# Performance work log

Hardware: AMD Instinct MI355X
Metric: run time of the kernel (lower is better)

The kernel has to match this reference:

```python
import jax, jax.numpy as jnp
import numpy as np

N_DETS = 50000
K_NEIGH = 32
E = N_DETS * K_NEIGH  # 1,600,000 pairs


def _linear_params(key, fan_in, fan_out):
    kw, kb = jax.random.split(key)
    scale = 1.0 / np.sqrt(fan_in)
    W = jax.random.uniform(kw, (fan_in, fan_out), jnp.float32, -scale, scale)
    b = jax.random.uniform(kb, (fan_out,), jnp.float32, -scale, scale)
    return W, b


def setup_inputs() -> dict:
    key = jax.random.key(0)
    ks = jax.random.split(key, 10)
    detFeatures = jax.random.normal(ks[0], (N_DETS, 128), jnp.float32)
    # each detection is the center of exactly K_NEIGH pairs (sorted segment ids)
    cIdxs = jnp.repeat(jnp.arange(N_DETS, dtype=jnp.int32), K_NEIGH)
    nIdxs = jax.random.randint(ks[1], (E,), 0, N_DETS, jnp.int32)
    pairFeatures = jax.random.normal(ks[2], (E, 32), jnp.float32)
    W1, b1 = _linear_params(ks[3], 128, 32)   # fc1: 128 -> 32
    Wp0, bp0 = _linear_params(ks[4], 96, 64)  # pwfeat fc 0: 3*32 -> 64
    Wp1, bp1 = _linear_params(ks[5], 64, 64)  # pwfeat fc 1
    Wq0, bq0 = _linear_params(ks[6], 64, 64)  # postmax fc 0
    Wq1, bq1 = _linear_params(ks[7], 64, 64)  # postmax fc 1
    Wo, bo = _linear_params(ks[8], 64, 128)   # output FC: 64 -> 128
    return {"detFeatures": detFeatures, "cIdxs": cIdxs, "nIdxs": nIdxs,
            "pairFeatures": pairFeatures,
            "W1": W1, "b1": b1, "Wp0": Wp0, "bp0": bp0, "Wp1": Wp1, "bp1": bp1,
            "Wq0": Wq0, "bq0": bq0, "Wq1": Wq1, "bq1": bq1, "Wo": Wo, "bo": bo}


def reference(detFeatures, cIdxs, nIdxs, pairFeatures,
              W1, b1, Wp0, bp0, Wp1, bp1, Wq0, bq0, Wq1, bq1, Wo, bo):
    relu = jax.nn.relu
    # fc1 shortcut reduce: [N,128] -> [N,32]
    f1 = relu(detFeatures @ W1 + b1)
    # gather center/neighbor feats and concat with pair feats: [E, 96]
    comb = jnp.concatenate([pairFeatures, f1[cIdxs], f1[nIdxs]], axis=1)
    h = relu(comb @ Wp0 + bp0)   # [E, 64]
    h = relu(h @ Wp1 + bp1)      # [E, 64]
    # per-detection segment max (replaces the Python loop in the original)
    pooled = jax.ops.segment_max(h, cIdxs, num_segments=detFeatures.shape[0])
    p = relu(pooled @ Wq0 + bq0)
    p = relu(p @ Wq1 + bq1)
    refined = p @ Wo + bo        # [N, 128]
    return relu(detFeatures + refined)
```

## Files before the change

### kernel.cpp

```cpp
#include <hip/hip_runtime.h>
#include <hip/hip_bf16.h>

typedef __attribute__((ext_vector_type(4))) float f32x4;
typedef __attribute__((ext_vector_type(8))) short bf16x8;
typedef __attribute__((ext_vector_type(2))) unsigned int uint2v;

#define N_DETS  50000
#define E_PAIRS 1600000
#define NB64    (E_PAIRS / 64)

__device__ __forceinline__ unsigned short f2bf(float f){
  union { float f; unsigned int u; } v; v.f = f;
  return (unsigned short)((v.u + 0x7FFFu + ((v.u >> 16) & 1u)) >> 16);
}

__device__ __forceinline__ bf16x8 pack8(f32x4 a, f32x4 b){
  union { unsigned int u[4]; bf16x8 v; } t;
  t.u[0] = (unsigned int)f2bf(a[0]) | ((unsigned int)f2bf(a[1]) << 16);
  t.u[1] = (unsigned int)f2bf(a[2]) | ((unsigned int)f2bf(a[3]) << 16);
  t.u[2] = (unsigned int)f2bf(b[0]) | ((unsigned int)f2bf(b[1]) << 16);
  t.u[3] = (unsigned int)f2bf(b[2]) | ((unsigned int)f2bf(b[3]) << 16);
  return t.v;
}

__global__ __launch_bounds__(256) void kA(const float* __restrict__ det,
                                          const float* __restrict__ W1,
                                          const float* __restrict__ b1,
                                          const float* __restrict__ Wp0,
                                          const float* __restrict__ Wp1,
                                          unsigned short* __restrict__ f1,
                                          unsigned short* __restrict__ wf){
  if (blockIdx.x < 40){
    int i = blockIdx.x * 256 + threadIdx.x;
    int f = i >> 9;
    int l = (i >> 3) & 63;
    int j = i & 7;
    int plc = l & 15, pq = l >> 4;
    float v;
    if (f < 12){
      int kt = f >> 2, ot = f & 3;
      v = Wp0[(kt*32 + pq*8 + j)*64 + ot*16 + plc];
    } else {
      int g = f - 12;
      int kt = g >> 2, n2 = g & 3;
      v = Wp1[(kt*32 + pq*8 + j)*64 + n2*16 + plc];
    }
    wf[i] = f2bf(v);
  }

  __shared__ float w[128*32];
  __shared__ float dt[16][132];
  const int t  = threadIdx.x;
  const int r0 = blockIdx.x * 16;
  {
    const f32x4* ws = reinterpret_cast<const f32x4*>(W1);
    #pragma unroll
    for (int i = 0; i < 4; ++i)
      reinterpret_cast<f32x4*>(w)[t + 256*i] = ws[t + 256*i];
    #pragma unroll
    for (int i = 0; i < 2; ++i){
      int idx = t + 256*i;
      int row = idx >> 5, c4 = (idx & 31) * 4;
      *reinterpret_cast<f32x4*>(&dt[row][c4]) =
        *reinterpret_cast<const f32x4*>(&det[(size_t)(r0+row)*128 + c4]);
    }
  }
  __syncthreads();
  const int r = t >> 4, c2 = (t & 15) * 2;
  float s0 = b1[c2], s1 = b1[c2 + 1];
  #pragma unroll 8
  for (int k = 0; k < 128; ++k){
    float d = dt[r][k];
    s0 = fmaf(d, w[k*32 + c2],     s0);
    s1 = fmaf(d, w[k*32 + c2 + 1], s1);
  }
  s0 = fmaxf(s0, 0.f); s1 = fmaxf(s1, 0.f);
  unsigned int pk = (unsigned int)f2bf(s0) | ((unsigned int)f2bf(s1) << 16);
  *reinterpret_cast<unsigned int*>(&f1[(size_t)(r0+r)*32 + c2]) = pk;
}

__global__ __launch_bounds__(256, 3) void kB(const float* __restrict__ pf,
                                             const int*   __restrict__ nIdxs,
                                             const unsigned short* __restrict__ f1,
                                             const unsigned short* __restrict__ wf,
                                             const float* __restrict__ bp0,
                                             const float* __restrict__ bp1,
                                             float* __restrict__ pooled){
  __shared__ __align__(16) unsigned short h1buf[4][4096];
  const int tid  = threadIdx.x;
  const int wid  = tid >> 6;
  const int lane = tid & 63;
  const int lc   = lane & 15;
  const int q    = lane >> 4;
  char* hb = reinterpret_cast<char*>(&h1buf[wid][0]);

  const bf16x8* wfv = reinterpret_cast<const bf16x8*>(wf);
  bf16x8 A0[3][4], B1w[2][4];
  #pragma unroll
  for (int kt = 0; kt < 3; ++kt)
    #pragma unroll
    for (int ot = 0; ot < 4; ++ot)
      A0[kt][ot] = wfv[(kt*4 + ot)*64 + lane];
  #pragma unroll
  for (int kt = 0; kt < 2; ++kt)
    #pragma unroll
    for (int n2 = 0; n2 < 4; ++n2)
      B1w[kt][n2] = wfv[(12 + kt*4 + n2)*64 + lane];

  f32x4 bb0[4];
  #pragma unroll
  for (int ot = 0; ot < 4; ++ot)
    bb0[ot] = *reinterpret_cast<const f32x4*>(&bp0[ot*16 + q*4]);
  const float bb1s = bp1[lane];

  const int nwaves = gridDim.x * 4;
  for (int b = blockIdx.x*4 + wid; b < NB64; b += nwaves){
    const int e0 = b * 64;

    int nid[4];
    #pragma unroll
    for (int et = 0; et < 4; ++et) nid[et] = nIdxs[e0 + et*16 + lc];
    bf16x8 f1n[4];
    #pragma unroll
    for (int et = 0; et < 4; ++et)
      f1n[et] = *reinterpret_cast<const bf16x8*>(&f1[(size_t)nid[et]*32 + q*8]);

    #pragma unroll
    for (int et = 0; et < 4; ++et){
      const int eg = e0 + et*16 + lc;
      f32x4 p0 = *reinterpret_cast<const f32x4*>(&pf[(size_t)eg*32 + q*8]);
      f32x4 p1 = *reinterpret_cast<const f32x4*>(&pf[(size_t)eg*32 + q*8 + 4]);
      const int c = (e0 >> 5) + (et >> 1);
      bf16x8 f1c = *reinterpret_cast<const bf16x8*>(&f1[(size_t)c*32 + q*8]);
      bf16x8 bfr0 = pack8(p0, p1);

      f32x4 acc[4];
      #pragma unroll
      for (int ot = 0; ot < 4; ++ot) acc[ot] = bb0[ot];
      #pragma unroll
      for (int ot = 0; ot < 4; ++ot){
        acc[ot] = __builtin_amdgcn_mfma_f32_16x16x32_bf16(A0[0][ot], bfr0,    acc[ot], 0,0,0);
        acc[ot] = __builtin_amdgcn_mfma_f32_16x16x32_bf16(A0[1][ot], f1c,     acc[ot], 0,0,0);
        acc[ot] = __builtin_amdgcn_mfma_f32_16x16x32_bf16(A0[2][ot], f1n[et], acc[ot], 0,0,0);
      }

      const int edge = et*16 + lc;
      const int swz  = (edge & 7) << 4;
      #pragma unroll
      for (int ot = 0; ot < 4; ++ot){
        f32x4 v = acc[ot];
        unsigned int lo = (unsigned int)f2bf(fmaxf(v[0],0.f)) | ((unsigned int)f2bf(fmaxf(v[1],0.f)) << 16);
        unsigned int hi = (unsigned int)f2bf(fmaxf(v[2],0.f)) | ((unsigned int)f2bf(fmaxf(v[3],0.f)) << 16);
        uint2v wv; wv[0] = lo; wv[1] = hi;
        *reinterpret_cast<uint2v*>(hb + ((edge*128 + ot*32 + q*8) ^ swz)) = wv;
      }
    }

    const int cbase = e0 >> 5;
    #pragma unroll
    for (int cen = 0; cen < 2; ++cen){
      const int eA = (2*cen)*16 + lc;
      const int eB = (2*cen + 1)*16 + lc;
      const int sw = (lc & 7) << 4;
      bf16x8 a0A = *reinterpret_cast<const bf16x8*>(hb + ((eA*128      + q*16) ^ sw));
      bf16x8 a1A = *reinterpret_cast<const bf16x8*>(hb + ((eA*128 + 64 + q*16) ^ sw));
      bf16x8 a0B = *reinterpret_cast<const bf16x8*>(hb + ((eB*128      + q*16) ^ sw));
      bf16x8 a1B = *reinterpret_cast<const bf16x8*>(hb + ((eB*128 + 64 + q*16) ^ sw));

      f32x4 accA[4], accB[4];
      #pragma unroll
      for (int n2 = 0; n2 < 4; ++n2){
        f32x4 z = {0.f, 0.f, 0.f, 0.f};
        accA[n2] = z; accB[n2] = z;
      }
      #pragma unroll
      for (int n2 = 0; n2 < 4; ++n2){
        accA[n2] = __builtin_amdgcn_mfma_f32_16x16x32_bf16(a0A, B1w[0][n2], accA[n2], 0,0,0);
        accA[n2] = __builtin_amdgcn_mfma_f32_16x16x32_bf16(a1A, B1w[1][n2], accA[n2], 0,0,0);
        accB[n2] = __builtin_amdgcn_mfma_f32_16x16x32_bf16(a0B, B1w[0][n2], accB[n2], 0,0,0);
        accB[n2] = __builtin_amdgcn_mfma_f32_16x16x32_bf16(a1B, B1w[1][n2], accB[n2], 0,0,0);
      }

      float s0n, s1n, s2n, s3n;
      #pragma unroll
      for (int n2 = 0; n2 < 4; ++n2){
        float m0 = fmaxf(fmaxf(accA[n2][0], accB[n2][0]), fmaxf(accA[n2][1], accB[n2][1]));
        float m1 = fmaxf(fmaxf(accA[n2][2], accB[n2][2]), fmaxf(accA[n2][3], accB[n2][3]));
        float mm = fmaxf(m0, m1);
        mm = fmaxf(mm, __shfl_xor(mm, 16));
        mm = fmaxf(mm, __shfl_xor(mm, 32));
        if (n2 == 0) s0n = mm; else if (n2 == 1) s1n = mm; else if (n2 == 2) s2n = mm; else s3n = mm;
      }
      float v01 = (q & 1) ? s1n : s0n;
      float v23 = (q & 1) ? s3n : s2n;
      float v   = (q & 2) ? v23 : v01;
      v = fmaxf(v + bb1s, 0.f);
      pooled[(size_t)(cbase + cen)*64 + lane] = v;
    }
  }
}

__global__ __launch_bounds__(256) void kC(const float* __restrict__ det,
                                          const float* __restrict__ pooled,
                                          const float* __restrict__ Wq0, const float* __restrict__ bq0,
                                          const float* __restrict__ Wq1, const float* __restrict__ bq1,
                                          const float* __restrict__ Wo,  const float* __restrict__ bo,
                                          float* __restrict__ out){
  __shared__ float pt[16*68];
  __shared__ float p1t[16*68];
  const int t  = threadIdx.x;
  const int r0 = blockIdx.x * 16;
  {
    int row = t >> 4, c4l = (t & 15) * 4;
    *reinterpret_cast<f32x4*>(&pt[row*68 + c4l]) =
      *reinterpret_cast<const f32x4*>(&pooled[(size_t)(r0+row)*64 + c4l]);
  }
  __syncthreads();
  const int r  = t >> 4;
  const int c4 = (t & 15) * 4;

  f32x4 a = *reinterpret_cast<const f32x4*>(&bq0[c4]);
  #pragma unroll 8
  for (int k = 0; k < 64; ++k){
    float pd = pt[r*68 + k];
    f32x4 wv = *reinterpret_cast<const f32x4*>(&Wq0[k*64 + c4]);
    a[0] = fmaf(pd, wv[0], a[0]); a[1] = fmaf(pd, wv[1], a[1]);
    a[2] = fmaf(pd, wv[2], a[2]); a[3] = fmaf(pd, wv[3], a[3]);
  }
  a[0]=fmaxf(a[0],0.f); a[1]=fmaxf(a[1],0.f); a[2]=fmaxf(a[2],0.f); a[3]=fmaxf(a[3],0.f);
  *reinterpret_cast<f32x4*>(&p1t[r*68 + c4]) = a;
  __syncthreads();

  f32x4 a2 = *reinterpret_cast<const f32x4*>(&bq1[c4]);
  #pragma unroll 8
  for (int k = 0; k < 64; ++k){
    float pd = p1t[r*68 + k];
    f32x4 wv = *reinterpret_cast<const f32x4*>(&Wq1[k*64 + c4]);
    a2[0] = fmaf(pd, wv[0], a2[0]); a2[1] = fmaf(pd, wv[1], a2[1]);
    a2[2] = fmaf(pd, wv[2], a2[2]); a2[3] = fmaf(pd, wv[3], a2[3]);
  }
  a2[0]=fmaxf(a2[0],0.f); a2[1]=fmaxf(a2[1],0.f); a2[2]=fmaxf(a2[2],0.f); a2[3]=fmaxf(a2[3],0.f);
  *reinterpret_cast<f32x4*>(&pt[r*68 + c4]) = a2;
  __syncthreads();

  f32x4 o0 = *reinterpret_cast<const f32x4*>(&bo[c4]);
  f32x4 o1 = *reinterpret_cast<const f32x4*>(&bo[64 + c4]);
  #pragma unroll 8
  for (int k = 0; k < 64; ++k){
    float pd = pt[r*68 + k];
    f32x4 wa = *reinterpret_cast<const f32x4*>(&Wo[k*128 + c4]);
    f32x4 wb = *reinterpret_cast<const f32x4*>(&Wo[k*128 + 64 + c4]);
    o0[0] = fmaf(pd, wa[0], o0[0]); o0[1] = fmaf(pd, wa[1], o0[1]);
    o0[2] = fmaf(pd, wa[2], o0[2]); o0[3] = fmaf(pd, wa[3], o0[3]);
    o1[0] = fmaf(pd, wb[0], o1[0]); o1[1] = fmaf(pd, wb[1], o1[1]);
    o1[2] = fmaf(pd, wb[2], o1[2]); o1[3] = fmaf(pd, wb[3], o1[3]);
  }
  const float* dr = &det[(size_t)(r0 + r) * 128];
  f32x4 d0 = *reinterpret_cast<const f32x4*>(&dr[c4]);
  f32x4 d1 = *reinterpret_cast<const f32x4*>(&dr[64 + c4]);
  f32x4 res0, res1;
  res0[0]=fmaxf(d0[0]+o0[0],0.f); res0[1]=fmaxf(d0[1]+o0[1],0.f);
  res0[2]=fmaxf(d0[2]+o0[2],0.f); res0[3]=fmaxf(d0[3]+o0[3],0.f);
  res1[0]=fmaxf(d1[0]+o1[0],0.f); res1[1]=fmaxf(d1[1]+o1[1],0.f);
  res1[2]=fmaxf(d1[2]+o1[2],0.f); res1[3]=fmaxf(d1[3]+o1[3],0.f);
  float* orow = &out[(size_t)(r0 + r) * 128];
  *reinterpret_cast<f32x4*>(&orow[c4])      = res0;
  *reinterpret_cast<f32x4*>(&orow[64 + c4]) = res1;
}

extern "C" void kernel_launch(void* const* d_in, const int* in_sizes, int n_in,
                              void* d_out, int out_size, void* d_ws, size_t ws_size,
                              hipStream_t stream){
  const float* det   = (const float*)d_in[0];
  const int*   nIdx  = (const int*)  d_in[2];
  const float* pfeat = (const float*)d_in[3];
  const float* W1    = (const float*)d_in[4];
  const float* b1    = (const float*)d_in[5];
  const float* Wp0   = (const float*)d_in[6];
  const float* bp0   = (const float*)d_in[7];
  const float* Wp1   = (const float*)d_in[8];
  const float* bp1   = (const float*)d_in[9];
  const float* Wq0   = (const float*)d_in[10];
  const float* bq0   = (const float*)d_in[11];
  const float* Wq1   = (const float*)d_in[12];
  const float* bq1   = (const float*)d_in[13];
  const float* Wo    = (const float*)d_in[14];
  const float* bo    = (const float*)d_in[15];
  float* out = (float*)d_out;

  unsigned short* f1 = (unsigned short*)d_ws;
  unsigned short* wf = (unsigned short*)((char*)d_ws + 3200000);
  float* pooled      = (float*)((char*)d_ws + 3225600);

  kA<<<N_DETS/16, 256, 0, stream>>>(det, W1, b1, Wp0, Wp1, f1, wf);
  kB<<<3125,      256, 0, stream>>>(pfeat, nIdx, f1, wf, bp0, bp1, pooled);
  kC<<<N_DETS/16, 256, 0, stream>>>(det, pooled, Wq0, bq0, Wq1, bq1, Wo, bo, out);
}
```

Measured before the change: 501.6 us.

## Prefetch next edge block in kB, use hardware bf16 pack, retile kA and kC

```diff
diff --git a/kernel.cpp b/kernel.cpp
--- a/kernel.cpp
+++ b/kernel.cpp
@@ -9,17 +9,23 @@
 #define E_PAIRS 1600000
 #define NB64    (E_PAIRS / 64)
 
+__device__ __forceinline__ unsigned int cvtpk(float lo, float hi){
+  unsigned int r;
+  asm("v_cvt_pk_bf16_f32 %0, %1, %2" : "=v"(r) : "v"(lo), "v"(hi));
+  return r;
+}
+
 __device__ __forceinline__ unsigned short f2bf(float f){
   union { float f; unsigned int u; } v; v.f = f;
   return (unsigned short)((v.u + 0x7FFFu + ((v.u >> 16) & 1u)) >> 16);
 }
 
-__device__ __forceinline__ bf16x8 pack8(f32x4 a, f32x4 b){
+__device__ __forceinline__ bf16x8 pack8v(f32x4 a, f32x4 b){
   union { unsigned int u[4]; bf16x8 v; } t;
-  t.u[0] = (unsigned int)f2bf(a[0]) | ((unsigned int)f2bf(a[1]) << 16);
-  t.u[1] = (unsigned int)f2bf(a[2]) | ((unsigned int)f2bf(a[3]) << 16);
-  t.u[2] = (unsigned int)f2bf(b[0]) | ((unsigned int)f2bf(b[1]) << 16);
-  t.u[3] = (unsigned int)f2bf(b[2]) | ((unsigned int)f2bf(b[3]) << 16);
+  t.u[0] = cvtpk(a[0], a[1]);
+  t.u[1] = cvtpk(a[2], a[3]);
+  t.u[2] = cvtpk(b[0], b[1]);
+  t.u[3] = cvtpk(b[2], b[3]);
   return t.v;
 }
 
@@ -49,34 +55,54 @@
   }
 
   __shared__ float w[128*32];
-  __shared__ float dt[16][132];
+  __shared__ float dt[64*132];
   const int t  = threadIdx.x;
-  const int r0 = blockIdx.x * 16;
+  const int r0 = blockIdx.x * 64;
   {
     const f32x4* ws = reinterpret_cast<const f32x4*>(W1);
     #pragma unroll
     for (int i = 0; i < 4; ++i)
       reinterpret_cast<f32x4*>(w)[t + 256*i] = ws[t + 256*i];
     #pragma unroll
-    for (int i = 0; i < 2; ++i){
+    for (int i = 0; i < 8; ++i){
       int idx = t + 256*i;
       int row = idx >> 5, c4 = (idx & 31) * 4;
-      *reinterpret_cast<f32x4*>(&dt[row][c4]) =
-        *reinterpret_cast<const f32x4*>(&det[(size_t)(r0+row)*128 + c4]);
+      int gr = r0 + row; if (gr > N_DETS-1) gr = N_DETS-1;
+      *reinterpret_cast<f32x4*>(&dt[row*132 + c4]) =
+        *reinterpret_cast<const f32x4*>(&det[(size_t)gr*128 + c4]);
     }
   }
   __syncthreads();
-  const int r = t >> 4, c2 = (t & 15) * 2;
-  float s0 = b1[c2], s1 = b1[c2 + 1];
-  #pragma unroll 8
-  for (int k = 0; k < 128; ++k){
-    float d = dt[r][k];
-    s0 = fmaf(d, w[k*32 + c2],     s0);
-    s1 = fmaf(d, w[k*32 + c2 + 1], s1);
-  }
-  s0 = fmaxf(s0, 0.f); s1 = fmaxf(s1, 0.f);
-  unsigned int pk = (unsigned int)f2bf(s0) | ((unsigned int)f2bf(s1) << 16);
-  *reinterpret_cast<unsigned int*>(&f1[(size_t)(r0+r)*32 + c2]) = pk;
+  const int rg = t >> 4;
+  const int c2 = (t & 15) * 2;
+  const float bw0 = b1[c2], bw1 = b1[c2 + 1];
+  float a0[4], a1[4];
+  #pragma unroll
+  for (int i = 0; i < 4; ++i){ a0[i] = bw0; a1[i] = bw1; }
+  for (int k4 = 0; k4 < 32; ++k4){
+    f32x4 dv[4];
+    #pragma unroll
+    for (int i = 0; i < 4; ++i)
+      dv[i] = *reinterpret_cast<const f32x4*>(&dt[(rg*4+i)*132 + k4*4]);
+    #pragma unroll
+    for (int kk = 0; kk < 4; ++kk){
+      float w0v = w[(k4*4+kk)*32 + c2];
+      float w1v = w[(k4*4+kk)*32 + c2 + 1];
+      #pragma unroll
+      for (int i = 0; i < 4; ++i){
+        a0[i] = fmaf(dv[i][kk], w0v, a0[i]);
+        a1[i] = fmaf(dv[i][kk], w1v, a1[i]);
+      }
+    }
+  }
+  #pragma unroll
+  for (int i = 0; i < 4; ++i){
+    int gr = r0 + rg*4 + i;
+    if (gr < N_DETS){
+      unsigned int pk = cvtpk(fmaxf(a0[i], 0.f), fmaxf(a1[i], 0.f));
+      *reinterpret_cast<unsigned int*>(&f1[(size_t)gr*32 + c2]) = pk;
+    }
+  }
 }
 
 __global__ __launch_bounds__(256, 3) void kB(const float* __restrict__ pf,
@@ -87,6 +113,8 @@
                                              const float* __restrict__ bp1,
                                              float* __restrict__ pooled){
   __shared__ __align__(16) unsigned short h1buf[4][4096];
+  __shared__ __align__(16) unsigned short b1w_lds[8*64*8];
+  __shared__ __align__(16) float bias0_lds[4*64*4];
   const int tid  = threadIdx.x;
   const int wid  = tid >> 6;
   const int lane = tid & 63;
@@ -95,68 +123,91 @@
   char* hb = reinterpret_cast<char*>(&h1buf[wid][0]);
 
   const bf16x8* wfv = reinterpret_cast<const bf16x8*>(wf);
-  bf16x8 A0[3][4], B1w[2][4];
+  bf16x8 A0[3][4];
   #pragma unroll
   for (int kt = 0; kt < 3; ++kt)
     #pragma unroll
     for (int ot = 0; ot < 4; ++ot)
       A0[kt][ot] = wfv[(kt*4 + ot)*64 + lane];
   #pragma unroll
-  for (int kt = 0; kt < 2; ++kt)
-    #pragma unroll
-    for (int n2 = 0; n2 < 4; ++n2)
-      B1w[kt][n2] = wfv[(12 + kt*4 + n2)*64 + lane];
-
-  f32x4 bb0[4];
+  for (int g = 0; g < 8; ++g)
+    *reinterpret_cast<bf16x8*>(&b1w_lds[(g*64 + lane)*8]) = wfv[(12 + g)*64 + lane];
   #pragma unroll
   for (int ot = 0; ot < 4; ++ot)
-    bb0[ot] = *reinterpret_cast<const f32x4*>(&bp0[ot*16 + q*4]);
+    *reinterpret_cast<f32x4*>(&bias0_lds[(ot*64 + lane)*4]) =
+      *reinterpret_cast<const f32x4*>(&bp0[ot*16 + q*4]);
   const float bb1s = bp1[lane];
 
-  const int nwaves = gridDim.x * 4;
-  for (int b = blockIdx.x*4 + wid; b < NB64; b += nwaves){
+  const int stride = gridDim.x * 4;
+  int b = blockIdx.x*4 + wid;
+
+  int nid[4]; f32x4 pfv[4][2]; bf16x8 f1cv[2];
+  {
     const int e0 = b * 64;
-
-    int nid[4];
     #pragma unroll
     for (int et = 0; et < 4; ++et) nid[et] = nIdxs[e0 + et*16 + lc];
+    #pragma unroll
+    for (int et = 0; et < 4; ++et){
+      pfv[et][0] = *reinterpret_cast<const f32x4*>(&pf[(size_t)(e0 + et*16 + lc)*32 + q*8]);
+      pfv[et][1] = *reinterpret_cast<const f32x4*>(&pf[(size_t)(e0 + et*16 + lc)*32 + q*8 + 4]);
+    }
+    #pragma unroll
+    for (int s = 0; s < 2; ++s)
+      f1cv[s] = *reinterpret_cast<const bf16x8*>(&f1[(size_t)(b*2 + s)*32 + q*8]);
+  }
+
+  while (b < NB64){
+    const int cbase = b * 2;
+
     bf16x8 f1n[4];
     #pragma unroll
     for (int et = 0; et < 4; ++et)
       f1n[et] = *reinterpret_cast<const bf16x8*>(&f1[(size_t)nid[et]*32 + q*8]);
+    bf16x8 bfr[4];
+    #pragma unroll
+    for (int et = 0; et < 4; ++et) bfr[et] = pack8v(pfv[et][0], pfv[et][1]);
+    bf16x8 f1c_cur0 = f1cv[0], f1c_cur1 = f1cv[1];
+
+    const int bn = b + stride;
+    const int bl = (bn < NB64) ? bn : b;
+    {
+      const int e0n = bl * 64;
+      #pragma unroll
+      for (int et = 0; et < 4; ++et) nid[et] = nIdxs[e0n + et*16 + lc];
+      #pragma unroll
+      for (int et = 0; et < 4; ++et){
+        pfv[et][0] = *reinterpret_cast<const f32x4*>(&pf[(size_t)(e0n + et*16 + lc)*32 + q*8]);
+        pfv[et][1] = *reinterpret_cast<const f32x4*>(&pf[(size_t)(e0n + et*16 + lc)*32 + q*8 + 4]);
+      }
+      #pragma unroll
+      for (int s = 0; s < 2; ++s)
+        f1cv[s] = *reinterpret_cast<const bf16x8*>(&f1[(size_t)(bl*2 + s)*32 + q*8]);
+    }
 
     #pragma unroll
     for (int et = 0; et < 4; ++et){
-      const int eg = e0 + et*16 + lc;
-      f32x4 p0 = *reinterpret_cast<const f32x4*>(&pf[(size_t)eg*32 + q*8]);
-      f32x4 p1 = *reinterpret_cast<const f32x4*>(&pf[(size_t)eg*32 + q*8 + 4]);
-      const int c = (e0 >> 5) + (et >> 1);
-      bf16x8 f1c = *reinterpret_cast<const bf16x8*>(&f1[(size_t)c*32 + q*8]);
-      bf16x8 bfr0 = pack8(p0, p1);
-
       f32x4 acc[4];
       #pragma unroll
-      for (int ot = 0; ot < 4; ++ot) acc[ot] = bb0[ot];
+      for (int ot = 0; ot < 4; ++ot)
+        acc[ot] = *reinterpret_cast<const f32x4*>(&bias0_lds[(ot*64 + lane)*4]);
+      bf16x8 f1cc = (et < 2) ? f1c_cur0 : f1c_cur1;
       #pragma unroll
       for (int ot = 0; ot < 4; ++ot){
-        acc[ot] = __builtin_amdgcn_mfma_f32_16x16x32_bf16(A0[0][ot], bfr0,    acc[ot], 0,0,0);
-        acc[ot] = __builtin_amdgcn_mfma_f32_16x16x32_bf16(A0[1][ot], f1c,     acc[ot], 0,0,0);
+        acc[ot] = __builtin_amdgcn_mfma_f32_16x16x32_bf16(A0[0][ot], bfr[et], acc[ot], 0,0,0);
+        acc[ot] = __builtin_amdgcn_mfma_f32_16x16x32_bf16(A0[1][ot], f1cc,    acc[ot], 0,0,0);
         acc[ot] = __builtin_amdgcn_mfma_f32_16x16x32_bf16(A0[2][ot], f1n[et], acc[ot], 0,0,0);
       }
-
       const int edge = et*16 + lc;
       const int swz  = (edge & 7) << 4;
       #pragma unroll
       for (int ot = 0; ot < 4; ++ot){
-        f32x4 v = acc[ot];
-        unsigned int lo = (unsigned int)f2bf(fmaxf(v[0],0.f)) | ((unsigned int)f2bf(fmaxf(v[1],0.f)) << 16);
-        unsigned int hi = (unsigned int)f2bf(fmaxf(v[2],0.f)) | ((unsigned int)f2bf(fmaxf(v[3],0.f)) << 16);
-        uint2v wv; wv[0] = lo; wv[1] = hi;
+        uint2v wv;
+        wv[0] = cvtpk(fmaxf(acc[ot][0], 0.f), fmaxf(acc[ot][1], 0.f));
+        wv[1] = cvtpk(fmaxf(acc[ot][2], 0.f), fmaxf(acc[ot][3], 0.f));
         *reinterpret_cast<uint2v*>(hb + ((edge*128 + ot*32 + q*8) ^ swz)) = wv;
       }
     }
 
-    const int cbase = e0 >> 5;
     #pragma unroll
     for (int cen = 0; cen < 2; ++cen){
       const int eA = (2*cen)*16 + lc;
@@ -175,10 +226,12 @@
       }
       #pragma unroll
       for (int n2 = 0; n2 < 4; ++n2){
-        accA[n2] = __builtin_amdgcn_mfma_f32_16x16x32_bf16(a0A, B1w[0][n2], accA[n2], 0,0,0);
-        accA[n2] = __builtin_amdgcn_mfma_f32_16x16x32_bf16(a1A, B1w[1][n2], accA[n2], 0,0,0);
-        accB[n2] = __builtin_amdgcn_mfma_f32_16x16x32_bf16(a0B, B1w[0][n2], accB[n2], 0,0,0);
-        accB[n2] = __builtin_amdgcn_mfma_f32_16x16x32_bf16(a1B, B1w[1][n2], accB[n2], 0,0,0);
+        bf16x8 bw0 = *reinterpret_cast<const bf16x8*>(&b1w_lds[((0*4 + n2)*64 + lane)*8]);
+        bf16x8 bw1 = *reinterpret_cast<const bf16x8*>(&b1w_lds[((1*4 + n2)*64 + lane)*8]);
+        accA[n2] = __builtin_amdgcn_mfma_f32_16x16x32_bf16(a0A, bw0, accA[n2], 0,0,0);
+        accA[n2] = __builtin_amdgcn_mfma_f32_16x16x32_bf16(a1A, bw1, accA[n2], 0,0,0);
+        accB[n2] = __builtin_amdgcn_mfma_f32_16x16x32_bf16(a0B, bw0, accB[n2], 0,0,0);
+        accB[n2] = __builtin_amdgcn_mfma_f32_16x16x32_bf16(a1B, bw1, accB[n2], 0,0,0);
       }
 
       float s0n, s1n, s2n, s3n;
@@ -197,6 +250,8 @@
       v = fmaxf(v + bb1s, 0.f);
       pooled[(size_t)(cbase + cen)*64 + lane] = v;
     }
+
+    b = bn;
   }
 }
 
@@ -206,66 +261,92 @@
                                           const float* __restrict__ Wq1, const float* __restrict__ bq1,
                                           const float* __restrict__ Wo,  const float* __restrict__ bo,
                                           float* __restrict__ out){
-  __shared__ float pt[16*68];
-  __shared__ float p1t[16*68];
+  __shared__ float w0s[64*64];
+  __shared__ float w1s[64*64];
+  __shared__ float pts[32*68];
+  __shared__ float p1s[32*68];
   const int t  = threadIdx.x;
-  const int r0 = blockIdx.x * 16;
+  const int r0 = blockIdx.x * 32;
   {
-    int row = t >> 4, c4l = (t & 15) * 4;
-    *reinterpret_cast<f32x4*>(&pt[row*68 + c4l]) =
-      *reinterpret_cast<const f32x4*>(&pooled[(size_t)(r0+row)*64 + c4l]);
+    const f32x4* s0 = reinterpret_cast<const f32x4*>(Wq0);
+    const f32x4* s1 = reinterpret_cast<const f32x4*>(Wq1);
+    #pragma unroll
+    for (int i = 0; i < 4; ++i) reinterpret_cast<f32x4*>(w0s)[t + 256*i] = s0[t + 256*i];
+    #pragma unroll
+    for (int i = 0; i < 4; ++i) reinterpret_cast<f32x4*>(w1s)[t + 256*i] = s1[t + 256*i];
+    #pragma unroll
+    for (int i = 0; i < 2; ++i){
+      int idx = t + 256*i;
+      int row = idx >> 4, c4l = (idx & 15) * 4;
+      int gr = r0 + row; if (gr > N_DETS-1) gr = N_DETS-1;
+      *reinterpret_cast<f32x4*>(&pts[row*68 + c4l]) =
+        *reinterpret_cast<const f32x4*>(&pooled[(size_t)gr*64 + c4l]);
+    }
   }
   __syncthreads();
-  const int r  = t >> 4;
+  const int rg = t >> 4;
   const int c4 = (t & 15) * 4;
-
-  f32x4 a = *reinterpret_cast<const f32x4*>(&bq0[c4]);
-  #pragma unroll 8
+  const int ra = rg*2, rb = rg*2 + 1;
+
+  f32x4 bq0v = *reinterpret_cast<const f32x4*>(&bq0[c4]);
+  f32x4 qa = bq0v, qb = bq0v;
   for (int k = 0; k < 64; ++k){
-    float pd = pt[r*68 + k];
-    f32x4 wv = *reinterpret_cast<const f32x4*>(&Wq0[k*64 + c4]);
-    a[0] = fmaf(pd, wv[0], a[0]); a[1] = fmaf(pd, wv[1], a[1]);
-    a[2] = fmaf(pd, wv[2], a[2]); a[3] = fmaf(pd, wv[3], a[3]);
-  }
-  a[0]=fmaxf(a[0],0.f); a[1]=fmaxf(a[1],0.f); a[2]=fmaxf(a[2],0.f); a[3]=fmaxf(a[3],0.f);
-  *reinterpret_cast<f32x4*>(&p1t[r*68 + c4]) = a;
+    f32x4 wv = *reinterpret_cast<const f32x4*>(&w0s[k*64 + c4]);
+    float pa = pts[ra*68 + k], pb = pts[rb*68 + k];
+    qa[0]=fmaf(pa,wv[0],qa[0]); qa[1]=fmaf(pa,wv[1],qa[1]); qa[2]=fmaf(pa,wv[2],qa[2]); qa[3]=fmaf(pa,wv[3],qa[3]);
+    qb[0]=fmaf(pb,wv[0],qb[0]); qb[1]=fmaf(pb,wv[1],qb[1]); qb[2]=fmaf(pb,wv[2],qb[2]); qb[3]=fmaf(pb,wv[3],qb[3]);
+  }
+  #pragma unroll
+  for (int j = 0; j < 4; ++j){ qa[j]=fmaxf(qa[j],0.f); qb[j]=fmaxf(qb[j],0.f); }
+  *reinterpret_cast<f32x4*>(&p1s[ra*68 + c4]) = qa;
+  *reinterpret_cast<f32x4*>(&p1s[rb*68 + c4]) = qb;
   __syncthreads();
 
-  f32x4 a2 = *reinterpret_cast<const f32x4*>(&bq1[c4]);
-  #pragma unroll 8
+  f32x4 bq1v = *reinterpret_cast<const f32x4*>(&bq1[c4]);
+  f32x4 ua = bq1v, ub = bq1v;
   for (int k = 0; k < 64; ++k){
-    float pd = p1t[r*68 + k];
-    f32x4 wv = *reinterpret_cast<const f32x4*>(&Wq1[k*64 + c4]);
-    a2[0] = fmaf(pd, wv[0], a2[0]); a2[1] = fmaf(pd, wv[1], a2[1]);
-    a2[2] = fmaf(pd, wv[2], a2[2]); a2[3] = fmaf(pd, wv[3], a2[3]);
-  }
-  a2[0]=fmaxf(a2[0],0.f); a2[1]=fmaxf(a2[1],0.f); a2[2]=fmaxf(a2[2],0.f); a2[3]=fmaxf(a2[3],0.f);
-  *reinterpret_cast<f32x4*>(&pt[r*68 + c4]) = a2;
+    f32x4 wv = *reinterpret_cast<const f32x4*>(&w1s[k*64 + c4]);
+    float pa = p1s[ra*68 + k], pb = p1s[rb*68 + k];
+    ua[0]=fmaf(pa,wv[0],ua[0]); ua[1]=fmaf(pa,wv[1],ua[1]); ua[2]=fmaf(pa,wv[2],ua[2]); ua[3]=fmaf(pa,wv[3],ua[3]);
+    ub[0]=fmaf(pb,wv[0],ub[0]); ub[1]=fmaf(pb,wv[1],ub[1]); ub[2]=fmaf(pb,wv[2],ub[2]); ub[3]=fmaf(pb,wv[3],ub[3]);
+  }
+  #pragma unroll
+  for (int j = 0; j < 4; ++j){ ua[j]=fmaxf(ua[j],0.f); ub[j]=fmaxf(ub[j],0.f); }
+  *reinterpret_cast<f32x4*>(&pts[ra*68 + c4]) = ua;
+  *reinterpret_cast<f32x4*>(&pts[rb*68 + c4]) = ub;
   __syncthreads();
 
-  f32x4 o0 = *reinterpret_cast<const f32x4*>(&bo[c4]);
-  f32x4 o1 = *reinterpret_cast<const f32x4*>(&bo[64 + c4]);
-  #pragma unroll 8
+  f32x4 boa = *reinterpret_cast<const f32x4*>(&bo[c4]);
+  f32x4 bob = *reinterpret_cast<const f32x4*>(&bo[64 + c4]);
+  f32x4 oa0 = boa, oa1 = bob, ob0 = boa, ob1 = bob;
   for (int k = 0; k < 64; ++k){
-    float pd = pt[r*68 + k];
     f32x4 wa = *reinterpret_cast<const f32x4*>(&Wo[k*128 + c4]);
     f32x4 wb = *reinterpret_cast<const f32x4*>(&Wo[k*128 + 64 + c4]);
-    o0[0] = fmaf(pd, wa[0], o0[0]); o0[1] = fmaf(pd, wa[1], o0[1]);
-    o0[2] = fmaf(pd, wa[2], o0[2]); o0[3] = fmaf(pd, wa[3], o0[3]);
-    o1[0] = fmaf(pd, wb[0], o1[0]); o1[1] = fmaf(pd, wb[1], o1[1]);
-    o1[2] = fmaf(pd, wb[2], o1[2]); o1[3] = fmaf(pd, wb[3], o1[3]);
-  }
-  const float* dr = &det[(size_t)(r0 + r) * 128];
-  f32x4 d0 = *reinterpret_cast<const f32x4*>(&dr[c4]);
-  f32x4 d1 = *reinterpret_cast<const f32x4*>(&dr[64 + c4]);
-  f32x4 res0, res1;
-  res0[0]=fmaxf(d0[0]+o0[0],0.f); res0[1]=fmaxf(d0[1]+o0[1],0.f);
-  res0[2]=fmaxf(d0[2]+o0[2],0.f); res0[3]=fmaxf(d0[3]+o0[3],0.f);
-  res1[0]=fmaxf(d1[0]+o1[0],0.f); res1[1]=fmaxf(d1[1]+o1[1],0.f);
-  res1[2]=fmaxf(d1[2]+o1[2],0.f); res1[3]=fmaxf(d1[3]+o1[3],0.f);
-  float* orow = &out[(size_t)(r0 + r) * 128];
-  *reinterpret_cast<f32x4*>(&orow[c4])      = res0;
-  *reinterpret_cast<f32x4*>(&orow[64 + c4]) = res1;
+    float pa = pts[ra*68 + k], pb = pts[rb*68 + k];
+    oa0[0]=fmaf(pa,wa[0],oa0[0]); oa0[1]=fmaf(pa,wa[1],oa0[1]); oa0[2]=fmaf(pa,wa[2],oa0[2]); oa0[3]=fmaf(pa,wa[3],oa0[3]);
+    oa1[0]=fmaf(pa,wb[0],oa1[0]); oa1[1]=fmaf(pa,wb[1],oa1[1]); oa1[2]=fmaf(pa,wb[2],oa1[2]); oa1[3]=fmaf(pa,wb[3],oa1[3]);
+    ob0[0]=fmaf(pb,wa[0],ob0[0]); ob0[1]=fmaf(pb,wa[1],ob0[1]); ob0[2]=fmaf(pb,wa[2],ob0[2]); ob0[3]=fmaf(pb,wa[3],ob0[3]);
+    ob1[0]=fmaf(pb,wb[0],ob1[0]); ob1[1]=fmaf(pb,wb[1],ob1[1]); ob1[2]=fmaf(pb,wb[2],ob1[2]); ob1[3]=fmaf(pb,wb[3],ob1[3]);
+  }
+  #pragma unroll
+  for (int rr = 0; rr < 2; ++rr){
+    int gr = r0 + rg*2 + rr;
+    if (gr < N_DETS){
+      const float* dr = &det[(size_t)gr * 128];
+      f32x4 d0 = *reinterpret_cast<const f32x4*>(&dr[c4]);
+      f32x4 d1 = *reinterpret_cast<const f32x4*>(&dr[64 + c4]);
+      f32x4 o0 = rr ? ob0 : oa0;
+      f32x4 o1 = rr ? ob1 : oa1;
+      f32x4 res0, res1;
+      res0[0]=fmaxf(d0[0]+o0[0],0.f); res0[1]=fmaxf(d0[1]+o0[1],0.f);
+      res0[2]=fmaxf(d0[2]+o0[2],0.f); res0[3]=fmaxf(d0[3]+o0[3],0.f);
+      res1[0]=fmaxf(d1[0]+o1[0],0.f); res1[1]=fmaxf(d1[1]+o1[1],0.f);
+      res1[2]=fmaxf(d1[2]+o1[2],0.f); res1[3]=fmaxf(d1[3]+o1[3],0.f);
+      float* orow = &out[(size_t)gr * 128];
+      *reinterpret_cast<f32x4*>(&orow[c4])      = res0;
+      *reinterpret_cast<f32x4*>(&orow[64 + c4]) = res1;
+    }
+  }
 }
 
 extern "C" void kernel_launch(void* const* d_in, const int* in_sizes, int n_in,
@@ -292,7 +373,7 @@
   unsigned short* wf = (unsigned short*)((char*)d_ws + 3200000);
   float* pooled      = (float*)((char*)d_ws + 3225600);
 
-  kA<<<N_DETS/16, 256, 0, stream>>>(det, W1, b1, Wp0, Wp1, f1, wf);
-  kB<<<3125,      256, 0, stream>>>(pfeat, nIdx, f1, wf, bp0, bp1, pooled);
-  kC<<<N_DETS/16, 256, 0, stream>>>(det, pooled, Wq0, bq0, Wq1, bq1, Wo, bo, out);
-}
+  kA<<<(N_DETS + 63)/64, 256, 0, stream>>>(det, W1, b1, Wp0, Wp1, f1, wf);
+  kB<<<768,             256, 0, stream>>>(pfeat, nIdx, f1, wf, bp0, bp1, pooled);
+  kC<<<(N_DETS + 31)/32, 256, 0, stream>>>(det, pooled, Wq0, bq0, Wq1, bq1, Wo, bo, out);
+}
```

Result: faster. 410.7 us (-18.1%).
